# Performance work log

Measured on AMD Instinct MI355X. Metric: run time of the kernel, lower is better.

## Reference

```python
import jax, jax.numpy as jnp
import numpy as np

BS, N, D = 2, 512, 128


def setup_inputs() -> dict:
    key = jax.random.key(0)
    ks = jax.random.split(key, 8)
    s = 1.0 / np.sqrt(D).astype(np.float32)
    x = jax.random.normal(ks[0], (BS, N, D), dtype=jnp.float32)
    Wq = jax.random.normal(ks[1], (D, D), dtype=jnp.float32) * s
    bq = jax.random.normal(ks[2], (D,), dtype=jnp.float32) * 0.01
    Wk = jax.random.normal(ks[3], (D, D), dtype=jnp.float32) * s
    bk = jax.random.normal(ks[4], (D,), dtype=jnp.float32) * 0.01
    Wv = jax.random.normal(ks[5], (D, D), dtype=jnp.float32) * s
    bv = jax.random.normal(ks[6], (D,), dtype=jnp.float32) * 0.01
    # position biases: [n, n]; randomized small so the pairwise path is non-trivial
    B = jax.random.normal(ks[7], (N, N), dtype=jnp.float32) * 0.02
    return {"x": x, "Wq": Wq, "bq": bq, "Wk": Wk, "bk": bk, "Wv": Wv, "bv": bv, "B": B}


def reference(x, Wq, bq, Wk, bk, Wv, bv, B):
    # x: [bs, n, d]
    q = x @ Wq + bq                      # [bs, n, d]
    k = x @ Wk + bk                      # [bs, n, d]
    v = x @ Wv + bv                      # [bs, n, d]
    # AFT-full: out[i] = sum_j exp(k_j + B_ij) * v_j / sum_j exp(k_j + B_ij)
    # Faithful to the torch broadcast: kb has shape [n_q, bs, n_k, d]
    kb = k[None, :, :, :] + B[:, None, :, None]
    m = jnp.max(kb, axis=2, keepdims=True)           # stable max over keys
    w = jnp.exp(kb - m)                              # [n_q, bs, n_k, d]
    num = jnp.einsum('ibjd,bjd->ibd', w, v)          # weighted sum over keys
    den = jnp.sum(w, axis=2)                         # [n_q, bs, d]
    out = num / den                                  # [n_q, bs, d]
    return jax.nn.sigmoid(q) * jnp.transpose(out, (1, 0, 2))
```

## Files before the change

kernel.cpp:

```cpp
#include <hip/hip_runtime.h>
#include <hip/hip_bf16.h>

#define BSZ 2
#define NN  512
#define DD  128


__global__ __launch_bounds__(128) void aft_k1(
    const float* __restrict__ x,
    const float* __restrict__ Wq, const float* __restrict__ bq,
    const float* __restrict__ Wk, const float* __restrict__ bk,
    const float* __restrict__ Wv, const float* __restrict__ bv,
    const float* __restrict__ Bm,
    float* __restrict__ qs, float* __restrict__ ekc, float* __restrict__ eb)
{
    const int blk = blockIdx.x;
    const int t   = threadIdx.x;

    if (blk < 128) {
        __shared__ float xs[8][DD];
        const int r0 = blk * 8;
        #pragma unroll
        for (int r = 0; r < 8; ++r)
            xs[r][t] = x[(size_t)(r0 + r) * DD + t];
        __syncthreads();

        float aq[8], ak[8], av[8];
        const float bqv = bq[t], bkv = bk[t], bvv = bv[t];
        #pragma unroll
        for (int r = 0; r < 8; ++r) { aq[r] = bqv; ak[r] = bkv; av[r] = bvv; }

        #pragma unroll 4
        for (int d = 0; d < DD; ++d) {
            const float wq = Wq[d * DD + t];
            const float wk = Wk[d * DD + t];
            const float wv = Wv[d * DD + t];
            #pragma unroll
            for (int r = 0; r < 8; ++r) {
                const float xv = xs[r][d];
                aq[r] = fmaf(xv, wq, aq[r]);
                ak[r] = fmaf(xv, wk, ak[r]);
                av[r] = fmaf(xv, wv, av[r]);
            }
        }

        #pragma unroll
        for (int r = 0; r < 8; ++r) {
            const int m  = r0 + r;
            const float ek = __expf(ak[r]);
            qs[(size_t)m * DD + t] = 1.0f / (1.0f + __expf(-aq[r]));
            float* base = ekc + (size_t)m * (2 * DD);
            base[t]      = ek * av[r];
            base[DD + t] = ek;
        }
    } else {
        const int e = blk - 128;
        const float4* s4 = (const float4*)Bm + (size_t)e * 256;
        float4*       d4 = (float4*)eb + (size_t)e * 256;
        #pragma unroll
        for (int r = 0; r < 2; ++r) {
            float4 v = s4[r * 128 + t];
            v.x = __expf(v.x); v.y = __expf(v.y);
            v.z = __expf(v.z); v.w = __expf(v.w);
            d4[r * 128 + t] = v;
        }
    }
}

__global__ __launch_bounds__(256) void aft_k2(
    const float* __restrict__ eb, const float* __restrict__ ekc,
    float* __restrict__ pnum, float* __restrict__ pden)
{
    const int blk = blockIdx.x;
    const int b   = blk & 1;
    const int it  = (blk >> 1) & 31;
    const int jc  = blk >> 6;
    const int c   = threadIdx.x;
    const int i0  = it * 16;
    const int j0  = jc * 128;

    const float* src = ekc + ((size_t)b * NN + j0) * (2 * DD) + c;
    const float* ebp = eb + (size_t)i0 * NN + j0;

    float acc[16];
    #pragma unroll
    for (int ii = 0; ii < 16; ++ii) acc[ii] = 0.0f;

    for (int j = 0; j < 128; j += 4) {
        const float w0 = src[0 * 2 * DD];
        const float w1 = src[1 * 2 * DD];
        const float w2 = src[2 * 2 * DD];
        const float w3 = src[3 * 2 * DD];
        src += 4 * 2 * DD;
        #pragma unroll
        for (int ii = 0; ii < 16; ++ii) {
            const float4 e = *(const float4*)(ebp + (size_t)ii * NN + j);
            acc[ii] = fmaf(e.w, w3, fmaf(e.z, w2, fmaf(e.y, w1, fmaf(e.x, w0, acc[ii]))));
        }
    }

    float*      dst = (c < DD) ? pnum : pden;
    const int   d   = c & (DD - 1);
    const size_t o  = ((size_t)jc * BSZ + b) * NN * DD + (size_t)i0 * DD + d;
    #pragma unroll
    for (int ii = 0; ii < 16; ++ii)
        dst[o + (size_t)ii * DD] = acc[ii];
}

__global__ __launch_bounds__(256) void aft_k3(
    const float* __restrict__ qs, const float* __restrict__ pnum,
    const float* __restrict__ pden, float* __restrict__ out)
{
    const int idx = blockIdx.x * 256 + threadIdx.x;
    const int S   = BSZ * NN * DD;
    const float n0 = pnum[idx] + pnum[idx + S] + pnum[idx + 2 * S] + pnum[idx + 3 * S];
    const float d0 = pden[idx] + pden[idx + S] + pden[idx + 2 * S] + pden[idx + 3 * S];
    out[idx] = qs[idx] * n0 / d0;
}

extern "C" void kernel_launch(void* const* d_in, const int* in_sizes, int n_in,
                              void* d_out, int out_size, void* d_ws, size_t ws_size,
                              hipStream_t stream) {
    const float* x  = (const float*)d_in[0];
    const float* Wq = (const float*)d_in[1];
    const float* bq = (const float*)d_in[2];
    const float* Wk = (const float*)d_in[3];
    const float* bk = (const float*)d_in[4];
    const float* Wv = (const float*)d_in[5];
    const float* bv = (const float*)d_in[6];
    const float* Bm = (const float*)d_in[7];
    float* out = (float*)d_out;

    float* qs   = (float*)d_ws;
    float* ekc  = qs   + (size_t)BSZ * NN * DD;
    float* eb   = ekc  + (size_t)BSZ * NN * 2 * DD;
    float* pnum = eb   + (size_t)NN * NN;
    float* pden = pnum + (size_t)4 * BSZ * NN * DD;

    aft_k1<<<dim3(384), dim3(128), 0, stream>>>(
        x, Wq, bq, Wk, bk, Wv, bv, Bm, qs, ekc, eb);
    aft_k2<<<dim3(256), dim3(256), 0, stream>>>(eb, ekc, pnum, pden);
    aft_k3<<<dim3(512), dim3(256), 0, stream>>>(qs, pnum, pden, out);
}
```

Measured before the change: 104.6 us.

## Fuse three AFT kernels into one cooperative kernel with grid syncs

Merges the projection/exp phase, the pairwise weighted-sum phase and the reduction phase into a single cooperative kernel of 256 blocks, separated by grid-wide barriers. Phase 1 is remapped so each 256-thread block computes 4 rows (2 per thread) and also exponentiates a slice of the bias matrix, so all three phases share one grid shape. This removes two kernel launches and the gaps between them, at the cost of grid-sync overhead and fewer rows per thread (less reuse of the weight loads) in the projection. A fallback to three separate launches runs if the cooperative launch fails.

```diff
diff --git a/kernel.cpp b/kernel.cpp
--- a/kernel.cpp
+++ b/kernel.cpp
@@ -1,12 +1,15 @@
 #include <hip/hip_runtime.h>
-#include <hip/hip_bf16.h>
+#include <hip/hip_cooperative_groups.h>
+
+namespace cg = cooperative_groups;
 
 #define BSZ 2
 #define NN  512
 #define DD  128
 
 
-__global__ __launch_bounds__(128) void aft_k1(
+__device__ __forceinline__ void phase1(
+    int blk, int tid,
     const float* __restrict__ x,
     const float* __restrict__ Wq, const float* __restrict__ bq,
     const float* __restrict__ Wk, const float* __restrict__ bk,
@@ -14,70 +17,58 @@
     const float* __restrict__ Bm,
     float* __restrict__ qs, float* __restrict__ ekc, float* __restrict__ eb)
 {
-    const int blk = blockIdx.x;
-    const int t   = threadIdx.x;
+    __shared__ float xs[4][DD];
+    const int r0 = blk * 4;
+    #pragma unroll
+    for (int u = 0; u < 2; ++u) {
+        const int idx = u * 256 + tid;
+        xs[idx >> 7][idx & 127] = x[(size_t)r0 * DD + idx];
+    }
+    __syncthreads();
 
-    if (blk < 128) {
-        __shared__ float xs[8][DD];
-        const int r0 = blk * 8;
-        #pragma unroll
-        for (int r = 0; r < 8; ++r)
-            xs[r][t] = x[(size_t)(r0 + r) * DD + t];
-        __syncthreads();
+    const int col = tid & 127;
+    const int rh  = (tid >> 7) * 2;
 
-        float aq[8], ak[8], av[8];
-        const float bqv = bq[t], bkv = bk[t], bvv = bv[t];
-        #pragma unroll
-        for (int r = 0; r < 8; ++r) { aq[r] = bqv; ak[r] = bkv; av[r] = bvv; }
+    float aq0 = bq[col], ak0 = bk[col], av0 = bv[col];
+    float aq1 = aq0, ak1 = ak0, av1 = av0;
+    #pragma unroll 4
+    for (int d = 0; d < DD; ++d) {
+        const float wq = Wq[d * DD + col];
+        const float wk = Wk[d * DD + col];
+        const float wv = Wv[d * DD + col];
+        const float x0 = xs[rh][d], x1 = xs[rh + 1][d];
+        aq0 = fmaf(x0, wq, aq0);  aq1 = fmaf(x1, wq, aq1);
+        ak0 = fmaf(x0, wk, ak0);  ak1 = fmaf(x1, wk, ak1);
+        av0 = fmaf(x0, wv, av0);  av1 = fmaf(x1, wv, av1);
+    }
+    const int m = r0 + rh;
+    const float ek0 = __expf(ak0), ek1 = __expf(ak1);
+    qs[(size_t)m * DD + col]       = 1.0f / (1.0f + __expf(-aq0));
+    qs[(size_t)(m + 1) * DD + col] = 1.0f / (1.0f + __expf(-aq1));
+    float* b0 = ekc + (size_t)m * (2 * DD);
+    b0[col]      = ek0 * av0;
+    b0[DD + col] = ek0;
+    float* b1 = ekc + (size_t)(m + 1) * (2 * DD);
+    b1[col]      = ek1 * av1;
+    b1[DD + col] = ek1;
 
-        #pragma unroll 4
-        for (int d = 0; d < DD; ++d) {
-            const float wq = Wq[d * DD + t];
-            const float wk = Wk[d * DD + t];
-            const float wv = Wv[d * DD + t];
-            #pragma unroll
-            for (int r = 0; r < 8; ++r) {
-                const float xv = xs[r][d];
-                aq[r] = fmaf(xv, wq, aq[r]);
-                ak[r] = fmaf(xv, wk, ak[r]);
-                av[r] = fmaf(xv, wv, av[r]);
-            }
-        }
-
-        #pragma unroll
-        for (int r = 0; r < 8; ++r) {
-            const int m  = r0 + r;
-            const float ek = __expf(ak[r]);
-            qs[(size_t)m * DD + t] = 1.0f / (1.0f + __expf(-aq[r]));
-            float* base = ekc + (size_t)m * (2 * DD);
-            base[t]      = ek * av[r];
-            base[DD + t] = ek;
-        }
-    } else {
-        const int e = blk - 128;
-        const float4* s4 = (const float4*)Bm + (size_t)e * 256;
-        float4*       d4 = (float4*)eb + (size_t)e * 256;
-        #pragma unroll
-        for (int r = 0; r < 2; ++r) {
-            float4 v = s4[r * 128 + t];
-            v.x = __expf(v.x); v.y = __expf(v.y);
-            v.z = __expf(v.z); v.w = __expf(v.w);
-            d4[r * 128 + t] = v;
-        }
-    }
+    const int i = blk * 256 + tid;
+    float4 v = ((const float4*)Bm)[i];
+    v.x = __expf(v.x); v.y = __expf(v.y); v.z = __expf(v.z); v.w = __expf(v.w);
+    ((float4*)eb)[i] = v;
 }
 
-__global__ __launch_bounds__(256) void aft_k2(
+__device__ __forceinline__ void phase2(
+    int blk, int tid,
     const float* __restrict__ eb, const float* __restrict__ ekc,
     float* __restrict__ pnum, float* __restrict__ pden)
 {
-    const int blk = blockIdx.x;
-    const int b   = blk & 1;
-    const int it  = (blk >> 1) & 31;
-    const int jc  = blk >> 6;
-    const int c   = threadIdx.x;
-    const int i0  = it * 16;
-    const int j0  = jc * 128;
+    const int b  = blk & 1;
+    const int it = (blk >> 1) & 31;
+    const int jc = blk >> 6;
+    const int c  = tid;
+    const int i0 = it * 16;
+    const int j0 = jc * 128;
 
     const float* src = ekc + ((size_t)b * NN + j0) * (2 * DD) + c;
     const float* ebp = eb + (size_t)i0 * NN + j0;
@@ -99,23 +90,71 @@
         }
     }
 
-    float*      dst = (c < DD) ? pnum : pden;
-    const int   d   = c & (DD - 1);
-    const size_t o  = ((size_t)jc * BSZ + b) * NN * DD + (size_t)i0 * DD + d;
+    float*       dst = (c < DD) ? pnum : pden;
+    const int    d   = c & (DD - 1);
+    const size_t o   = ((size_t)jc * BSZ + b) * NN * DD + (size_t)i0 * DD + d;
     #pragma unroll
     for (int ii = 0; ii < 16; ++ii)
         dst[o + (size_t)ii * DD] = acc[ii];
 }
 
-__global__ __launch_bounds__(256) void aft_k3(
+__device__ __forceinline__ void phase3(
+    int blk, int tid,
     const float* __restrict__ qs, const float* __restrict__ pnum,
     const float* __restrict__ pden, float* __restrict__ out)
 {
-    const int idx = blockIdx.x * 256 + threadIdx.x;
-    const int S   = BSZ * NN * DD;
-    const float n0 = pnum[idx] + pnum[idx + S] + pnum[idx + 2 * S] + pnum[idx + 3 * S];
-    const float d0 = pden[idx] + pden[idx + S] + pden[idx + 2 * S] + pden[idx + 3 * S];
-    out[idx] = qs[idx] * n0 / d0;
+    const int S = BSZ * NN * DD;
+    #pragma unroll
+    for (int u = 0; u < 2; ++u) {
+        const int idx = blk * 512 + u * 256 + tid;
+        const float n0 = pnum[idx] + pnum[idx + S] + pnum[idx + 2 * S] + pnum[idx + 3 * S];
+        const float d0 = pden[idx] + pden[idx + S] + pden[idx + 2 * S] + pden[idx + 3 * S];
+        out[idx] = qs[idx] * n0 / d0;
+    }
+}
+
+__global__ __launch_bounds__(256) void aft_fused(
+    const float* __restrict__ x,
+    const float* __restrict__ Wq, const float* __restrict__ bq,
+    const float* __restrict__ Wk, const float* __restrict__ bk,
+    const float* __restrict__ Wv, const float* __restrict__ bv,
+    const float* __restrict__ Bm,
+    float* __restrict__ qs, float* __restrict__ ekc, float* __restrict__ eb,
+    float* __restrict__ pnum, float* __restrict__ pden,
+    float* __restrict__ out)
+{
+    cg::grid_group grid = cg::this_grid();
+    const int blk = blockIdx.x, tid = threadIdx.x;
+    phase1(blk, tid, x, Wq, bq, Wk, bk, Wv, bv, Bm, qs, ekc, eb);
+    grid.sync();
+    phase2(blk, tid, eb, ekc, pnum, pden);
+    grid.sync();
+    phase3(blk, tid, qs, pnum, pden, out);
+}
+
+__global__ __launch_bounds__(256) void aft_p1(
+    const float* __restrict__ x,
+    const float* __restrict__ Wq, const float* __restrict__ bq,
+    const float* __restrict__ Wk, const float* __restrict__ bk,
+    const float* __restrict__ Wv, const float* __restrict__ bv,
+    const float* __restrict__ Bm,
+    float* __restrict__ qs, float* __restrict__ ekc, float* __restrict__ eb)
+{
+    phase1(blockIdx.x, threadIdx.x, x, Wq, bq, Wk, bk, Wv, bv, Bm, qs, ekc, eb);
+}
+
+__global__ __launch_bounds__(256) void aft_p2(
+    const float* __restrict__ eb, const float* __restrict__ ekc,
+    float* __restrict__ pnum, float* __restrict__ pden)
+{
+    phase2(blockIdx.x, threadIdx.x, eb, ekc, pnum, pden);
+}
+
+__global__ __launch_bounds__(256) void aft_p3(
+    const float* __restrict__ qs, const float* __restrict__ pnum,
+    const float* __restrict__ pden, float* __restrict__ out)
+{
+    phase3(blockIdx.x, threadIdx.x, qs, pnum, pden, out);
 }
 
 extern "C" void kernel_launch(void* const* d_in, const int* in_sizes, int n_in,
@@ -137,8 +176,17 @@
     float* pnum = eb   + (size_t)NN * NN;
     float* pden = pnum + (size_t)4 * BSZ * NN * DD;
 
-    aft_k1<<<dim3(384), dim3(128), 0, stream>>>(
-        x, Wq, bq, Wk, bk, Wv, bv, Bm, qs, ekc, eb);
-    aft_k2<<<dim3(256), dim3(256), 0, stream>>>(eb, ekc, pnum, pden);
-    aft_k3<<<dim3(512), dim3(256), 0, stream>>>(qs, pnum, pden, out);
+    void* args[] = { (void*)&x, (void*)&Wq, (void*)&bq, (void*)&Wk, (void*)&bk,
+                     (void*)&Wv, (void*)&bv, (void*)&Bm, (void*)&qs, (void*)&ekc,
+                     (void*)&eb, (void*)&pnum, (void*)&pden, (void*)&out };
+
+    hipError_t err = hipLaunchCooperativeKernel(
+        (const void*)aft_fused, dim3(256), dim3(256), args, 0, stream);
+
+    if (err != hipSuccess) {
+        aft_p1<<<dim3(256), dim3(256), 0, stream>>>(
+            x, Wq, bq, Wk, bk, Wv, bv, Bm, qs, ekc, eb);
+        aft_p2<<<dim3(256), dim3(256), 0, stream>>>(eb, ekc, pnum, pden);
+        aft_p3<<<dim3(256), dim3(256), 0, stream>>>(qs, pnum, pden, out);
+    }
 }
```

After: 173.3 us. 65.7% more time.
